# Optimization experiments

Measured on AMD Instinct MI355X. Metric: run time of the kernel, lower is better.

The kernel has to match this reference:

```python
import jax, jax.numpy as jnp
import numpy as np

B, H, W, DIN = 512, 14, 14, 512
EDIM, K = 64, 256
GRID = 2  # code grid -> code_seq_len = 4


def setup_inputs() -> dict:
    key = jax.random.key(0)
    ks = jax.random.split(key, 12)
    def lin(k, fin, fout):
        return jax.random.normal(k, (fin, fout), jnp.float32) / np.sqrt(fin).astype(np.float32)
    return {
        "features_t0": jax.random.normal(ks[0], (B, H, W, DIN), jnp.float32),
        "features_t1": jax.random.normal(ks[1], (B, H, W, DIN), jnp.float32),
        "enc_w1": lin(ks[2], DIN, 2 * EDIM), "enc_b1": jnp.zeros((2 * EDIM,), jnp.float32),
        "enc_w2": lin(ks[3], 2 * EDIM, EDIM), "enc_b2": jnp.zeros((EDIM,), jnp.float32),
        "dec_w1": lin(ks[4], EDIM, 2 * EDIM), "dec_b1": jnp.zeros((2 * EDIM,), jnp.float32),
        "dec_w2": lin(ks[5], 2 * EDIM, DIN), "dec_b2": jnp.zeros((DIN,), jnp.float32),
        "codebook": jax.random.normal(ks[6], (K, EDIM), jnp.float32),
    }


def reference(features_t0, features_t1, enc_w1, enc_b1, enc_w2, enc_b2,
              dec_w1, dec_b1, dec_w2, dec_b2, codebook):
    # eval-mode forward (no EMA update / data init)
    delta = features_t1 - features_t0                       # [B,H,W,DIN]
    h = jax.nn.gelu(delta @ enc_w1 + enc_b1, approximate=False)
    e = h @ enc_w2 + enc_b2                                 # [B,H,W,EDIM]
    # AdaptiveAvgPool2d((2,2)) on 14x14 == exact 7x7 block mean
    bh, bw = H // GRID, W // GRID
    pooled = e.reshape(B, GRID, bh, GRID, bw, EDIM).mean(axis=(2, 4))  # [B,2,2,EDIM]
    enc = pooled.reshape(B, GRID * GRID, EDIM)              # [B,4,EDIM]

    flat = enc.reshape(-1, EDIM)                            # [B*4, EDIM]
    d2 = ((flat ** 2).sum(-1, keepdims=True)
          - 2.0 * flat @ codebook.T
          + (codebook ** 2).sum(-1))                        # [N,K]
    idx = jnp.argmin(d2, axis=1)                            # [N]
    quantized = codebook[idx]                               # [N,EDIM]

    commitment_loss = jnp.mean((jax.lax.stop_gradient(quantized) - flat) ** 2)
    q_st = flat + jax.lax.stop_gradient(quantized - flat)   # straight-through

    n_tok = flat.shape[0]
    avg_probs = jnp.zeros((K,), flat.dtype).at[idx].add(1.0) / n_tok
    perplexity = jnp.exp(-jnp.sum(avg_probs * jnp.log(avg_probs + 1e-10)))

    q = q_st.reshape(B, GRID * GRID, EDIM)
    hd = jax.nn.gelu(q @ dec_w1 + dec_b1, approximate=False)
    dec = hd @ dec_w2 + dec_b2                              # [B,4,DIN]
    sp = dec.reshape(B, GRID, GRID, DIN).transpose(0, 3, 1, 2)  # [B,DIN,2,2]
    # bilinear, align_corners=False (half-pixel centers, matches jax.image.resize)
    up = jax.image.resize(sp, (B, DIN, H, W), method="bilinear")
    decoded = up.transpose(0, 2, 3, 1)                      # [B,H,W,DIN]

    indices = idx.reshape(B, GRID * GRID)
    return decoded, perplexity, commitment_loss, indices
```

## Files before the change

### kernel.cpp

```cpp
#include <hip/hip_runtime.h>
#include <math.h>

#define N_TOKENS   2048
#define DECODED_SZ 51380224

typedef __attribute__((ext_vector_type(8)))  short bf16x8;
typedef __attribute__((ext_vector_type(16))) float f32x16;

__device__ __forceinline__ float gelu_exact(float x) {
    return 0.5f * x * (1.0f + erff(x * 0.70710678118654752440f));
}

__device__ __forceinline__ unsigned int f2bf(float x) {
    unsigned int u = __float_as_uint(x);
    return (u + 0x7fffu + ((u >> 16) & 1u)) >> 16;
}
__device__ __forceinline__ float bf2f(unsigned int b) {
    return __uint_as_float(b << 16);
}

__device__ __forceinline__ unsigned int cvt_pk_bf16(float a, float b) {
    unsigned int p;
    asm("v_cvt_pk_bf16_f32 %0, %1, %2" : "=v"(p) : "v"(a), "v"(b));
    return p;
}
__device__ __forceinline__ void split_pair(float a, float b,
                                           unsigned int& hi, unsigned int& lo) {
    hi = cvt_pk_bf16(a, b);
    const float ra = a - __uint_as_float(hi << 16);
    const float rb = b - __uint_as_float(hi & 0xffff0000u);
    lo = cvt_pk_bf16(ra, rb);
}

__global__ __launch_bounds__(256) void k0_prep_w1(
    const float* __restrict__ w1,
    unsigned short* __restrict__ bth, unsigned short* __restrict__ btl,
    float* __restrict__ hist)
{
    if (blockIdx.x == 0) {
        hist[threadIdx.x] = 0.0f;
        if (threadIdx.x == 0) hist[256] = 0.0f;
    }

    const int i  = blockIdx.x * 256 + threadIdx.x;
    const int n  = i >> 6;
    const int kg = i & 63;
    const int k0i = kg * 8;

    unsigned int h[8], lo[8];
#pragma unroll
    for (int j = 0; j < 8; ++j) {
        float v = w1[(k0i + j) * 128 + n];
        h[j]  = f2bf(v);
        lo[j] = f2bf(v - bf2f(h[j]));
    }
    const int idx = (k0i >> 5) * 4096 + n * 32 + (k0i & 31);
    uint4 hv, lv;
    hv.x = h[0]  | (h[1] << 16);  hv.y = h[2]  | (h[3] << 16);
    hv.z = h[4]  | (h[5] << 16);  hv.w = h[6]  | (h[7] << 16);
    lv.x = lo[0] | (lo[1] << 16); lv.y = lo[2] | (lo[3] << 16);
    lv.z = lo[4] | (lo[5] << 16); lv.w = lo[6] | (lo[7] << 16);
    *reinterpret_cast<uint4*>(bth + idx) = hv;
    *reinterpret_cast<uint4*>(btl + idx) = lv;
}

__global__ __launch_bounds__(512, 4) void k1_enc_pool(
    const float* __restrict__ t0, const float* __restrict__ t1,
    const unsigned short* __restrict__ bth, const unsigned short* __restrict__ btl,
    const float* __restrict__ b1,
    float* __restrict__ part)
{
    __shared__ unsigned short sAh[2][4096];
    __shared__ unsigned short sAl[2][4096];
    __shared__ float sR[4][4][128];

    const int t    = threadIdx.x;
    const int bid  = blockIdx.x;
    const int b    = bid >> 1;
    const int half = bid & 1;
    const int l     = t & 63;
    const int w     = t >> 6;
    const int wm    = w >> 1;
    const int wn    = w & 1;
    const int lan31 = l & 31;
    const int h     = l >> 5;

    const float4* __restrict__ t0v = reinterpret_cast<const float4*>(t0);
    const float4* __restrict__ t1v = reinterpret_cast<const float4*>(t1);

    int aG[2], aW[2];
#pragma unroll
    for (int j = 0; j < 2; ++j) {
        const int i = t + j * 512;
        const int r = i >> 3, f = i & 7;
        const int rg = b * 196 + min(half * 128 + r, 195);
        aG[j] = rg * 128 + f;
        aW[j] = r * 32 + 8 * ((f >> 1) ^ (r & 3)) + 4 * (f & 1);
    }

    int arOff[2];
    int brOff[2][2];
    {
        const int r = wm * 32 + lan31;
#pragma unroll
        for (int ks = 0; ks < 2; ++ks)
            arOff[ks] = r * 32 + 8 * ((2 * ks + h) ^ (r & 3));
#pragma unroll
        for (int ni = 0; ni < 2; ++ni) {
            const int c = (wn * 2 + ni) * 32 + lan31;
#pragma unroll
            for (int ks = 0; ks < 2; ++ks)
                brOff[ni][ks] = c * 32 + ks * 16 + h * 8;
        }
    }
    const bool tile_ok = (half * 4 + wm) < 7;

    f32x16 acc[2] = {};

    float4 p0a, p0b, p1a, p1b;

    p1a = t1v[aG[0]]; p0a = t0v[aG[0]];
    p1b = t1v[aG[1]]; p0b = t0v[aG[1]];

#pragma unroll 2
    for (int kc = 0; kc < 16; ++kc) {
        unsigned short* __restrict__ ah = sAh[kc & 1];
        unsigned short* __restrict__ al = sAl[kc & 1];

        {
            unsigned int h0, l0, h1, l1;
            split_pair(p1a.x - p0a.x, p1a.y - p0a.y, h0, l0);
            split_pair(p1a.z - p0a.z, p1a.w - p0a.w, h1, l1);
            *reinterpret_cast<uint2*>(ah + aW[0]) = make_uint2(h0, h1);
            *reinterpret_cast<uint2*>(al + aW[0]) = make_uint2(l0, l1);
            split_pair(p1b.x - p0b.x, p1b.y - p0b.y, h0, l0);
            split_pair(p1b.z - p0b.z, p1b.w - p0b.w, h1, l1);
            *reinterpret_cast<uint2*>(ah + aW[1]) = make_uint2(h0, h1);
            *reinterpret_cast<uint2*>(al + aW[1]) = make_uint2(l0, l1);
        }
        __syncthreads();

        if (kc < 15) {
            const int g = (kc + 1) * 8;
            p1a = t1v[aG[0] + g]; p0a = t0v[aG[0] + g];
            p1b = t1v[aG[1] + g]; p0b = t0v[aG[1] + g];
        }
        __builtin_amdgcn_sched_barrier(0);

        if (tile_ok) {
            const unsigned short* __restrict__ bhp = bth + kc * 4096;
            const unsigned short* __restrict__ blp = btl + kc * 4096;
#pragma unroll
            for (int ks = 0; ks < 2; ++ks) {
                const bf16x8 fah = *reinterpret_cast<const bf16x8*>(ah + arOff[ks]);
                const bf16x8 fal = *reinterpret_cast<const bf16x8*>(al + arOff[ks]);
#pragma unroll
                for (int ni = 0; ni < 2; ++ni) {
                    const bf16x8 fbh = *reinterpret_cast<const bf16x8*>(bhp + brOff[ni][ks]);
                    const bf16x8 fbl = *reinterpret_cast<const bf16x8*>(blp + brOff[ni][ks]);
                    acc[ni] = __builtin_amdgcn_mfma_f32_32x32x16_bf16(
                        fah, fbh, acc[ni], 0, 0, 0);
                    acc[ni] = __builtin_amdgcn_mfma_f32_32x32x16_bf16(
                        fah, fbl, acc[ni], 0, 0, 0);
                    acc[ni] = __builtin_amdgcn_mfma_f32_32x32x16_bf16(
                        fal, fbh, acc[ni], 0, 0, 0);
                }
            }
        }
    }

    float tokacc[2][4] = {};
#pragma unroll
    for (int ni = 0; ni < 2; ++ni) {
        const int col = (wn * 2 + ni) * 32 + lan31;
        const float bias = b1[col];
#pragma unroll
        for (int reg = 0; reg < 16; ++reg) {
            const int rl = wm * 32 + (reg & 3) + 8 * (reg >> 2) + 4 * h;
            const int rg = half * 128 + rl;
            if (rg < 196) {
                const float v = gelu_exact(acc[ni][reg] + bias);
                const int py = rg / 14, px = rg % 14;
                const int tok = ((py >= 7) ? 2 : 0) + ((px >= 7) ? 1 : 0);
                tokacc[ni][tok] += v;
            }
        }
    }
#pragma unroll
    for (int ni = 0; ni < 2; ++ni)
#pragma unroll
        for (int tok = 0; tok < 4; ++tok)
            tokacc[ni][tok] += __shfl_xor(tokacc[ni][tok], 32);
    if (h == 0) {
#pragma unroll
        for (int ni = 0; ni < 2; ++ni)
#pragma unroll
            for (int tok = 0; tok < 4; ++tok)
                sR[wm][tok][wn * 64 + ni * 32 + lan31] = tokacc[ni][tok];
    }
    __syncthreads();
    {
        const int tok = t >> 7, col = t & 127;
        part[bid * 512 + tok * 128 + col] =
            sR[0][tok][col] + sR[1][tok][col] + sR[2][tok][col] + sR[3][tok][col];
    }
}

__global__ __launch_bounds__(256, 2) void k2_mid(
    const float* __restrict__ part,
    const float* __restrict__ w2,  const float* __restrict__ b2,
    const float* __restrict__ cb,
    const float* __restrict__ dw1, const float* __restrict__ db1,
    const float* __restrict__ dw2, const float* __restrict__ db2,
    float* __restrict__ dec, float* __restrict__ hist, float* __restrict__ commit,
    float* __restrict__ out_idx)
{
    __shared__ float sCB[256 * 66];
    __shared__ float ph[4 * 128];
    __shared__ float es[4 * 64];
    __shared__ float hd[4 * 128];
    __shared__ float rd[256];
    __shared__ int   ri[256];
    __shared__ int   idxs[4];
    __shared__ float dms[4];

    const int t   = threadIdx.x;
    const int tk0 = blockIdx.x * 4;

    if (t < 128) {
        const float4 x = reinterpret_cast<const float4*>(
            part + (blockIdx.x * 2 + 0) * 512)[t];
        const float4 y = reinterpret_cast<const float4*>(
            part + (blockIdx.x * 2 + 1) * 512)[t];
        float4 s;
        s.x = (x.x + y.x) * (1.0f / 49.0f);
        s.y = (x.y + y.y) * (1.0f / 49.0f);
        s.z = (x.z + y.z) * (1.0f / 49.0f);
        s.w = (x.w + y.w) * (1.0f / 49.0f);
        reinterpret_cast<float4*>(ph)[t] = s;
    }
    for (int i = t; i < 16384; i += 256) {
        int row = i >> 6, k = i & 63;
        sCB[row * 66 + k] = cb[i];
    }
    __syncthreads();

    {
        const int j = t & 63, tok = t >> 6;
        float a = b2[j];
        const float* phr = ph + tok * 128;
#pragma unroll 8
        for (int k = 0; k < 128; ++k)
            a = fmaf(phr[k], w2[k * 64 + j], a);
        es[tok * 64 + j] = a;
    }
    __syncthreads();

    {
        const int tok = t >> 6, c8 = t & 63;
        float2 ev[32];
#pragma unroll
        for (int k = 0; k < 32; ++k)
            ev[k] = *reinterpret_cast<const float2*>(es + tok * 64 + 2 * k);
        float dmin = 3.4e38f; int imin = 0;
#pragma unroll
        for (int cc = 0; cc < 4; ++cc) {
            const int c = c8 + cc * 64;
            const float* cr = sCB + c * 66;
            float d = 0.f;
#pragma unroll
            for (int k = 0; k < 32; ++k) {
                float2 c2 = *reinterpret_cast<const float2*>(cr + 2 * k);
                float d0 = ev[k].x - c2.x;
                float d1 = ev[k].y - c2.y;
                d = fmaf(d0, d0, d);
                d = fmaf(d1, d1, d);
            }
            if (d < dmin || (d == dmin && c < imin)) { dmin = d; imin = c; }
        }
        rd[t] = dmin; ri[t] = imin;
    }
    __syncthreads();
    for (int s = 32; s > 0; s >>= 1) {
        if ((t & 63) < s) {
            float dn = rd[t + s]; int in = ri[t + s];
            if (dn < rd[t] || (dn == rd[t] && in < ri[t])) { rd[t] = dn; ri[t] = in; }
        }
        __syncthreads();
    }
    if ((t & 63) == 0) {
        const int tok = t >> 6;
        idxs[tok] = ri[t];
        dms[tok]  = rd[t];
        out_idx[tk0 + tok] = (float)ri[t];
        atomicAdd(&hist[ri[t]], 1.0f);
    }
    __syncthreads();
    if (t == 0) {
        float s = dms[0] + dms[1] + dms[2] + dms[3];
        atomicAdd(commit, s);
    }

    {
        const int j = t & 127, half = t >> 7;
        const float bj = db1[j];
        float a0 = bj, a1 = bj;
        const float* q0 = sCB + idxs[half * 2 + 0] * 66;
        const float* q1 = sCB + idxs[half * 2 + 1] * 66;
#pragma unroll 4
        for (int k = 0; k < 64; ++k) {
            const float wv = dw1[k * 128 + j];
            a0 = fmaf(q0[k], wv, a0);
            a1 = fmaf(q1[k], wv, a1);
        }
        hd[(half * 2 + 0) * 128 + j] = gelu_exact(a0);
        hd[(half * 2 + 1) * 128 + j] = gelu_exact(a1);
    }
    __syncthreads();

    {
        float a0[4], a1[4];
        const float bb0 = db2[t], bb1 = db2[t + 256];
#pragma unroll
        for (int q = 0; q < 4; ++q) { a0[q] = bb0; a1[q] = bb1; }
#pragma unroll 2
        for (int j = 0; j < 128; ++j) {
            const float w0 = dw2[j * 512 + t];
            const float w1v = dw2[j * 512 + 256 + t];
#pragma unroll
            for (int q = 0; q < 4; ++q) {
                const float h = hd[q * 128 + j];
                a0[q] = fmaf(h, w0, a0[q]);
                a1[q] = fmaf(h, w1v, a1[q]);
            }
        }
#pragma unroll
        for (int q = 0; q < 4; ++q) {
            dec[(tk0 + q) * 512 + t]       = a0[q];
            dec[(tk0 + q) * 512 + 256 + t] = a1[q];
        }
    }
}

__global__ __launch_bounds__(256, 4) void k3_upsample(
    const float* __restrict__ dec, float* __restrict__ out,
    const float* __restrict__ hist, const float* __restrict__ commit,
    float* __restrict__ out2)
{
    __shared__ float  sdec[4 * 512];
    __shared__ float4 wts[196];
    __shared__ int4   offs[196];
    const int b = blockIdx.x, t = threadIdx.x;

    if (b == 512) {
        __shared__ float red[256];
        float p = hist[t] * (1.0f / 2048.0f);
        red[t] = p * logf(p + 1e-10f);
        __syncthreads();
        for (int s = 128; s > 0; s >>= 1) {
            if (t < s) red[t] += red[t + s];
            __syncthreads();
        }
        if (t == 0) {
            out2[0] = expf(-red[0]);
            out2[1] = commit[0] * (1.0f / 131072.0f);
        }
        return;
    }

    for (int i = t; i < 512; i += 256)
        reinterpret_cast<float4*>(sdec)[i] =
            reinterpret_cast<const float4*>(dec + b * 2048)[i];
    if (t < 196) {
        const int y = t / 14, x = t % 14;
        const float sy = (y + 0.5f) * (1.0f / 7.0f) - 0.5f;
        const float sx = (x + 0.5f) * (1.0f / 7.0f) - 0.5f;
        const int iy = (int)floorf(sy), ix = (int)floorf(sx);
        const float fy = sy - (float)iy, fx = sx - (float)ix;
        const int y0 = min(max(iy, 0), 1), y1 = min(max(iy + 1, 0), 1);
        const int x0 = min(max(ix, 0), 1), x1 = min(max(ix + 1, 0), 1);
        float4 w;
        w.x = (1.f - fy) * (1.f - fx); w.y = (1.f - fy) * fx;
        w.z = fy * (1.f - fx);         w.w = fy * fx;
        wts[t] = w;
        int4 o;
        o.x = (y0 * 2 + x0) * 128; o.y = (y0 * 2 + x1) * 128;
        o.z = (y1 * 2 + x0) * 128; o.w = (y1 * 2 + x1) * 128;
        offs[t] = o;
    }
    __syncthreads();

    const float4* s4 = reinterpret_cast<const float4*>(sdec);
    float4* o4 = reinterpret_cast<float4*>(out) + b * 25088;
    const int c4 = t & 127, ph2 = t >> 7;

#pragma unroll 2
    for (int it = 0; it < 98; ++it) {
        const int pos = ph2 + it * 2;
        const float4 w = wts[pos];
        const int4   o = offs[pos];
        const float4 v00 = s4[o.x + c4];
        const float4 v01 = s4[o.y + c4];
        const float4 v10 = s4[o.z + c4];
        const float4 v11 = s4[o.w + c4];
        float4 r;
        r.x = w.x * v00.x + w.y * v01.x + w.z * v10.x + w.w * v11.x;
        r.y = w.x * v00.y + w.y * v01.y + w.z * v10.y + w.w * v11.y;
        r.z = w.x * v00.z + w.y * v01.z + w.z * v10.z + w.w * v11.z;
        r.w = w.x * v00.w + w.y * v01.w + w.z * v10.w + w.w * v11.w;
        o4[pos * 128 + c4] = r;
    }
}

extern "C" void kernel_launch(void* const* d_in, const int* in_sizes, int n_in,
                              void* d_out, int out_size, void* d_ws, size_t ws_size,
                              hipStream_t stream)
{
    const float* t0  = (const float*)d_in[0];
    const float* t1  = (const float*)d_in[1];
    const float* w1  = (const float*)d_in[2];
    const float* b1  = (const float*)d_in[3];
    const float* w2  = (const float*)d_in[4];
    const float* b2  = (const float*)d_in[5];
    const float* dw1 = (const float*)d_in[6];
    const float* db1 = (const float*)d_in[7];
    const float* dw2 = (const float*)d_in[8];
    const float* db2 = (const float*)d_in[9];
    const float* cb  = (const float*)d_in[10];

    float* out = (float*)d_out;
    float* ws  = (float*)d_ws;

    float* part   = ws;
    float* dec    = ws + 524288;
    float* hist   = ws + 1572864;
    float* commit = ws + 1573120;

    unsigned short* bth = (unsigned short*)(ws + 524288);
    unsigned short* btl = (unsigned short*)(ws + 524288 + 32768);

    k0_prep_w1<<<32, 256, 0, stream>>>(w1, bth, btl, hist);
    k1_enc_pool<<<1024, 512, 0, stream>>>(t0, t1, bth, btl, b1, part);
    k2_mid<<<512, 256, 0, stream>>>(part, w2, b2, cb, dw1, db1, dw2, db2,
                                    dec, hist, commit, out + DECODED_SZ + 2);
    k3_upsample<<<513, 256, 0, stream>>>(dec, out, hist, commit, out + DECODED_SZ);
}
```

Measured before the change: 621.1 us.

## Split encoder tiles into quarter-image 256-thread blocks with padded LDS rows

```diff
diff --git a/kernel.cpp b/kernel.cpp
--- a/kernel.cpp
+++ b/kernel.cpp
@@ -64,20 +64,20 @@
     *reinterpret_cast<uint4*>(btl + idx) = lv;
 }
 
-__global__ __launch_bounds__(512, 4) void k1_enc_pool(
+__global__ __launch_bounds__(256, 6) void k1_enc_pool(
     const float* __restrict__ t0, const float* __restrict__ t1,
     const unsigned short* __restrict__ bth, const unsigned short* __restrict__ btl,
     const float* __restrict__ b1,
     float* __restrict__ part)
 {
-    __shared__ unsigned short sAh[2][4096];
-    __shared__ unsigned short sAl[2][4096];
-    __shared__ float sR[4][4][128];
+    __shared__ unsigned short sAh[2][2560];
+    __shared__ unsigned short sAl[2][2560];
+    __shared__ float sR[2][4][128];
 
     const int t    = threadIdx.x;
     const int bid  = blockIdx.x;
-    const int b    = bid >> 1;
-    const int half = bid & 1;
+    const int b    = bid >> 2;
+    const int q    = bid & 3;
     const int l     = t & 63;
     const int w     = t >> 6;
     const int wm    = w >> 1;
@@ -91,11 +91,11 @@
     int aG[2], aW[2];
 #pragma unroll
     for (int j = 0; j < 2; ++j) {
-        const int i = t + j * 512;
+        const int i = t + j * 256;
         const int r = i >> 3, f = i & 7;
-        const int rg = b * 196 + min(half * 128 + r, 195);
+        const int rg = b * 196 + min(q * 64 + r, 195);
         aG[j] = rg * 128 + f;
-        aW[j] = r * 32 + 8 * ((f >> 1) ^ (r & 3)) + 4 * (f & 1);
+        aW[j] = r * 40 + 8 * ((f >> 1) ^ ((r >> 3) & 3)) + 4 * (f & 1);
     }
 
     int arOff[2];
@@ -104,7 +104,7 @@
         const int r = wm * 32 + lan31;
 #pragma unroll
         for (int ks = 0; ks < 2; ++ks)
-            arOff[ks] = r * 32 + 8 * ((2 * ks + h) ^ (r & 3));
+            arOff[ks] = r * 40 + 8 * ((2 * ks + h) ^ ((r >> 3) & 3));
 #pragma unroll
         for (int ni = 0; ni < 2; ++ni) {
             const int c = (wn * 2 + ni) * 32 + lan31;
@@ -113,7 +113,7 @@
                 brOff[ni][ks] = c * 32 + ks * 16 + h * 8;
         }
     }
-    const bool tile_ok = (half * 4 + wm) < 7;
+    const bool tile_ok = (q * 2 + wm) * 32 < 196;
 
     f32x16 acc[2] = {};
 
@@ -177,7 +177,7 @@
 #pragma unroll
         for (int reg = 0; reg < 16; ++reg) {
             const int rl = wm * 32 + (reg & 3) + 8 * (reg >> 2) + 4 * h;
-            const int rg = half * 128 + rl;
+            const int rg = q * 64 + rl;
             if (rg < 196) {
                 const float v = gelu_exact(acc[ni][reg] + bias);
                 const int py = rg / 14, px = rg % 14;
@@ -199,10 +199,9 @@
                 sR[wm][tok][wn * 64 + ni * 32 + lan31] = tokacc[ni][tok];
     }
     __syncthreads();
-    {
-        const int tok = t >> 7, col = t & 127;
-        part[bid * 512 + tok * 128 + col] =
-            sR[0][tok][col] + sR[1][tok][col] + sR[2][tok][col] + sR[3][tok][col];
+    for (int i = t; i < 512; i += 256) {
+        const int tok = i >> 7, col = i & 127;
+        part[bid * 512 + tok * 128 + col] = sR[0][tok][col] + sR[1][tok][col];
     }
 }
 
@@ -228,15 +227,15 @@
     const int tk0 = blockIdx.x * 4;
 
     if (t < 128) {
-        const float4 x = reinterpret_cast<const float4*>(
-            part + (blockIdx.x * 2 + 0) * 512)[t];
-        const float4 y = reinterpret_cast<const float4*>(
-            part + (blockIdx.x * 2 + 1) * 512)[t];
-        float4 s;
-        s.x = (x.x + y.x) * (1.0f / 49.0f);
-        s.y = (x.y + y.y) * (1.0f / 49.0f);
-        s.z = (x.z + y.z) * (1.0f / 49.0f);
-        s.w = (x.w + y.w) * (1.0f / 49.0f);
+        float4 s = make_float4(0.f, 0.f, 0.f, 0.f);
+#pragma unroll
+        for (int qq = 0; qq < 4; ++qq) {
+            const float4 x = reinterpret_cast<const float4*>(
+                part + (blockIdx.x * 4 + qq) * 512)[t];
+            s.x += x.x; s.y += x.y; s.z += x.z; s.w += x.w;
+        }
+        s.x *= (1.0f / 49.0f); s.y *= (1.0f / 49.0f);
+        s.z *= (1.0f / 49.0f); s.w *= (1.0f / 49.0f);
         reinterpret_cast<float4*>(ph)[t] = s;
     }
     for (int i = t; i < 16384; i += 256) {
@@ -322,22 +321,22 @@
         float a0[4], a1[4];
         const float bb0 = db2[t], bb1 = db2[t + 256];
 #pragma unroll
-        for (int q = 0; q < 4; ++q) { a0[q] = bb0; a1[q] = bb1; }
+        for (int qq = 0; qq < 4; ++qq) { a0[qq] = bb0; a1[qq] = bb1; }
 #pragma unroll 2
         for (int j = 0; j < 128; ++j) {
             const float w0 = dw2[j * 512 + t];
             const float w1v = dw2[j * 512 + 256 + t];
 #pragma unroll
-            for (int q = 0; q < 4; ++q) {
-                const float h = hd[q * 128 + j];
-                a0[q] = fmaf(h, w0, a0[q]);
-                a1[q] = fmaf(h, w1v, a1[q]);
+            for (int qq = 0; qq < 4; ++qq) {
+                const float h = hd[qq * 128 + j];
+                a0[qq] = fmaf(h, w0, a0[qq]);
+                a1[qq] = fmaf(h, w1v, a1[qq]);
             }
         }
 #pragma unroll
-        for (int q = 0; q < 4; ++q) {
-            dec[(tk0 + q) * 512 + t]       = a0[q];
-            dec[(tk0 + q) * 512 + 256 + t] = a1[q];
+        for (int qq = 0; qq < 4; ++qq) {
+            dec[(tk0 + qq) * 512 + t]       = a0[qq];
+            dec[(tk0 + qq) * 512 + 256 + t] = a1[qq];
         }
     }
 }
@@ -432,15 +431,14 @@
     float* ws  = (float*)d_ws;
 
     float* part   = ws;
-    float* dec    = ws + 524288;
-    float* hist   = ws + 1572864;
-    float* commit = ws + 1573120;
-
-    unsigned short* bth = (unsigned short*)(ws + 524288);
-    unsigned short* btl = (unsigned short*)(ws + 524288 + 32768);
+    float* dec    = ws;
+    unsigned short* bth = (unsigned short*)(ws + 1048576);
+    unsigned short* btl = (unsigned short*)(ws + 1048576 + 32768);
+    float* hist   = ws + 1114112;
+    float* commit = ws + 1114368;
 
     k0_prep_w1<<<32, 256, 0, stream>>>(w1, bth, btl, hist);
-    k1_enc_pool<<<1024, 512, 0, stream>>>(t0, t1, bth, btl, b1, part);
+    k1_enc_pool<<<2048, 256, 0, stream>>>(t0, t1, bth, btl, b1, part);
     k2_mid<<<512, 256, 0, stream>>>(part, w2, b2, cb, dw1, db1, dw2, db2,
                                     dec, hist, commit, out + DECODED_SZ + 2);
     k3_upsample<<<513, 256, 0, stream>>>(dec, out, hist, commit, out + DECODED_SZ);
```

New measurement: 1.075 ms. 1.73x slower.
